# Kernel optimization log

Measured on AMD Instinct MI355X. Metric: run time of the kernel, lower is better.

## Reference

```python
import jax, jax.numpy as jnp
import numpy as np

B, S, D = 32, 2048, 1024
H = 8
D_ATTN = 256
D_HEAD = D_ATTN // H          # 32
D_HEAD_OUT = D // H           # 128
SOFTMAX_TEMP = 1.0


def setup_inputs() -> dict:
    key = jax.random.key(0)
    k0, k1, k2, k3, k4 = jax.random.split(key, 5)
    features = jax.random.normal(k0, (B, S, D), dtype=jnp.float32)
    # truncated-normal(std=0.01) init approximated with scaled normal
    w1 = jax.random.normal(k1, (H, D, D_HEAD), dtype=jnp.float32) * 0.01
    b1 = jax.random.normal(k2, (H, D_HEAD), dtype=jnp.float32) * 0.01
    w2 = jax.random.normal(k3, (H, D_HEAD, D_HEAD_OUT), dtype=jnp.float32) * 0.01
    b2 = jax.random.normal(k4, (H, D_HEAD_OUT), dtype=jnp.float32) * 0.01
    return {"features": features, "w1": w1, "b1": b1, "w2": w2, "b2": b2}


def reference(features, w1, b1, w2, b2):
    Bc, Sc, Dc = features.shape
    # per-head first projection: [B,H,S,d_head]
    h = jnp.einsum('bsd,hde->bhse', features, w1) + b1[None, :, None, :]
    h = jax.nn.gelu(h, approximate=False)  # torch nn.GELU default is exact erf
    # second projection: [B,H,S,d_head_out]
    logits = jnp.einsum('bhse,heo->bhso', h, w2) + b2[None, :, None, :]
    # softmax over seq dim (axis=2)
    smw = jax.nn.softmax(logits / SOFTMAX_TEMP, axis=2)
    # [B,H,S,D/H] -> [B,S,H,D/H] -> [B,S,D]
    smw = smw.transpose(0, 2, 1, 3).reshape(Bc, Sc, Dc)
    return (features * smw).sum(axis=1)  # [B,D]
```

## Files before the change

### kernel.cpp

```cpp
#include <hip/hip_runtime.h>
#include <hip/hip_bf16.h>
#include <math.h>

#define S_  2048
#define D_  1024

typedef __attribute__((ext_vector_type(8))) short short8;
typedef __attribute__((ext_vector_type(4))) float f32x4;

static __device__ __forceinline__ short f2bf(float x) {
    return __builtin_bit_cast(short, __float2bfloat16(x));
}
static __device__ __forceinline__ float bf2f(unsigned short s) {
    unsigned int u = ((unsigned int)s) << 16;
    return __builtin_bit_cast(float, u);
}

__device__ __forceinline__ void gl_lds16(const void* g, void* l) {
    __builtin_amdgcn_global_load_lds(
        (const __attribute__((address_space(1))) unsigned int*)g,
        (__attribute__((address_space(3))) unsigned int*)l, 16, 0, 0);
}

__global__ void prep_w1(const float* __restrict__ w1, short* __restrict__ w1p) {
    int tid = blockIdx.x * 256 + threadIdx.x;
    int lane = tid & 63;
    int fragid = tid >> 6;
    int cf = fragid & 15, ks = fragid >> 4;
    int col = cf * 16 + (lane & 15);
    int h = col >> 5, e = col & 31;
    int d0 = ks * 32 + (lane >> 4) * 8;
    short8 v;
#pragma unroll
    for (int r = 0; r < 8; ++r)
        v[r] = f2bf(w1[((size_t)h * D_ + (d0 + r)) * 32 + e]);
    *(short8*)(w1p + (size_t)tid * 8) = v;
}

__global__ void prep_w2(const float* __restrict__ w2, short* __restrict__ w2p) {
    int tid = blockIdx.x * 256 + threadIdx.x;
    int lane = tid & 63;
    int fragid = tid >> 6;
    int cf2 = fragid & 7, h = fragid >> 3;
    int o = cf2 * 16 + (lane & 15);
    int e0 = (lane >> 4) * 8;
    short8 v;
#pragma unroll
    for (int r = 0; r < 8; ++r)
        v[r] = f2bf(w2[((size_t)h * 32 + (e0 + r)) * 128 + o]);
    *(short8*)(w2p + (size_t)tid * 8) = v;
}

__global__ __launch_bounds__(256, 2) void gemm1(
        const float* __restrict__ feat,
        const short* __restrict__ w1p,
        const float* __restrict__ b1,
        short* __restrict__ hact)
{
    __shared__ short hstage[4][32][264];

    const int tid = threadIdx.x;
    const int wv = tid >> 6;
    const int lane = tid & 63;
    const int lr = lane & 15;
    const int lg = lane >> 4;
    const size_t mw = ((size_t)blockIdx.x * 4 + wv) * 32;

    const f32x4* A0 = (const f32x4*)(feat + (mw + lr) * D_);
    const f32x4* A1 = (const f32x4*)(feat + (mw + 16 + lr) * D_);
    const short8* Bp = (const short8*)w1p;

    const f32x4 vzero = {0.f, 0.f, 0.f, 0.f};
    f32x4 acc[2][16];
#pragma unroll
    for (int i = 0; i < 2; ++i)
#pragma unroll
        for (int j = 0; j < 16; ++j) acc[i][j] = vzero;

    f32x4 p0 = A0[lg * 2], p1 = A0[lg * 2 + 1];
    f32x4 p2 = A1[lg * 2], p3 = A1[lg * 2 + 1];

    for (int ks = 0; ks < 32; ++ks) {
        short8 af0, af1;
        af0[0] = f2bf(p0.x); af0[1] = f2bf(p0.y); af0[2] = f2bf(p0.z); af0[3] = f2bf(p0.w);
        af0[4] = f2bf(p1.x); af0[5] = f2bf(p1.y); af0[6] = f2bf(p1.z); af0[7] = f2bf(p1.w);
        af1[0] = f2bf(p2.x); af1[1] = f2bf(p2.y); af1[2] = f2bf(p2.z); af1[3] = f2bf(p2.w);
        af1[4] = f2bf(p3.x); af1[5] = f2bf(p3.y); af1[6] = f2bf(p3.z); af1[7] = f2bf(p3.w);
        if (ks < 31) {
            const int o = (ks + 1) * 8 + lg * 2;
            p0 = A0[o]; p1 = A0[o + 1];
            p2 = A1[o]; p3 = A1[o + 1];
        }
        const short8* Bk = Bp + (size_t)ks * 16 * 64 + lane;
#pragma unroll
        for (int cf = 0; cf < 16; ++cf) {
            short8 b = Bk[cf * 64];
            acc[0][cf] = __builtin_amdgcn_mfma_f32_16x16x32_bf16(af0, b, acc[0][cf], 0, 0, 0);
            acc[1][cf] = __builtin_amdgcn_mfma_f32_16x16x32_bf16(af1, b, acc[1][cf], 0, 0, 0);
        }
    }

#pragma unroll
    for (int cf = 0; cf < 16; ++cf) {
        const int col = cf * 16 + lr;
        const float bias = b1[col];
#pragma unroll
        for (int a = 0; a < 2; ++a)
#pragma unroll
        for (int r = 0; r < 4; ++r) {
            const int row = a * 16 + lg * 4 + r;
            float x = acc[a][cf][r] + bias;
            float g = 0.5f * x * (1.0f + erff(x * 0.70710678118654752f));
            hstage[wv][row][col] = f2bf(g);
        }
    }
#pragma unroll
    for (int it = 0; it < 16; ++it) {
        const int idx = it * 64 + lane;
        const int row = idx >> 5;
        const int c8 = idx & 31;
        short8 v = *(const short8*)(&hstage[wv][row][c8 * 8]);
        *(short8*)(hact + (mw + row) * 256 + c8 * 8) = v;
    }
}

__global__ __launch_bounds__(256) void gemm2w(
        const short* __restrict__ hact,
        const float* __restrict__ feat,
        const short* __restrict__ w2p,
        const float* __restrict__ b2,
        float* __restrict__ pnum,
        float* __restrict__ pden)
{
    __shared__ __align__(16) char lds[41216];
    short* hstage = (short*)lds;
    unsigned short* Est = (unsigned short*)(lds + 8192);

    const int tid = threadIdx.x;
    const int wv = tid >> 6;
    const int lane = tid & 63;
    const int lr = lane & 15;
    const int lg = lane >> 4;
    const size_t m0 = (size_t)blockIdx.x * 16;

#pragma unroll
    for (int j = 0; j < 2; ++j)
        gl_lds16(hact + m0 * 256 + (size_t)(j * 256 + tid) * 8,
                 hstage + (j * 256 + wv * 64) * 8);

    float bias2[16];
#pragma unroll
    for (int cf = 0; cf < 16; ++cf)
        bias2[cf] = b2[(2 * wv + (cf >> 3)) * 128 + (cf & 7) * 16 + lr];

    __syncthreads();

    short8 ah0 = *(const short8*)(hstage + lr * 256 + (2 * wv + 0) * 32 + lg * 8);
    short8 ah1 = *(const short8*)(hstage + lr * 256 + (2 * wv + 1) * 32 + lg * 8);
    const f32x4 vzero = {0.f, 0.f, 0.f, 0.f};
#pragma unroll
    for (int cf = 0; cf < 16; ++cf) {
        const int h = 2 * wv + (cf >> 3);
        short8 bw = *(const short8*)(w2p + ((size_t)(h * 8 + (cf & 7)) * 64 + lane) * 8);
        f32x4 c = vzero;
        c = __builtin_amdgcn_mfma_f32_16x16x32_bf16((cf < 8) ? ah0 : ah1, bw, c, 0, 0, 0);
        const int colL = wv * 256 + (cf >> 3) * 128 + (cf & 7) * 16 + lr;
#pragma unroll
        for (int r = 0; r < 4; ++r) {
            float e = __expf(c[r] + bias2[cf]);
            Est[(lg * 4 + r) * 1032 + colL] = (unsigned short)f2bf(e);
        }
    }
    __syncthreads();

    const int c0 = tid * 4;
    f32x4 nacc = vzero, dacc = vzero;
    const float* fb = feat + m0 * D_ + c0;
#pragma unroll
    for (int row = 0; row < 16; ++row) {
        f32x4 fv = *(const f32x4*)(fb + (size_t)row * D_);
        unsigned long long ev = *(const unsigned long long*)(Est + row * 1032 + c0);
        f32x4 e;
        e.x = bf2f((unsigned short)(ev));
        e.y = bf2f((unsigned short)(ev >> 16));
        e.z = bf2f((unsigned short)(ev >> 32));
        e.w = bf2f((unsigned short)(ev >> 48));
        dacc += e;
        nacc += fv * e;
    }
    const size_t pb = (size_t)blockIdx.x * 1024 + c0;
    *(f32x4*)(pnum + pb) = nacc;
    *(f32x4*)(pden + pb) = dacc;
}

__global__ __launch_bounds__(256) void finalize3(
        const float* __restrict__ pnum,
        const float* __restrict__ pden,
        float* __restrict__ out)
{
    const int idx = blockIdx.x * 256 + threadIdx.x;
    const int b = idx >> 10;
    const int d = idx & 1023;
    const size_t base = (size_t)b * 128 * 1024 + d;
    float n = 0.f, dn = 0.f;
    for (int j = 0; j < 128; ++j) {
        n  += pnum[base + (size_t)j * 1024];
        dn += pden[base + (size_t)j * 1024];
    }
    out[idx] = n / dn;
}

extern "C" void kernel_launch(void* const* d_in, const int* in_sizes, int n_in,
                              void* d_out, int out_size, void* d_ws, size_t ws_size,
                              hipStream_t stream) {
    (void)in_sizes; (void)n_in; (void)out_size; (void)ws_size;
    const float* feat = (const float*)d_in[0];
    const float* w1   = (const float*)d_in[1];
    const float* b1   = (const float*)d_in[2];
    const float* w2   = (const float*)d_in[3];
    const float* b2   = (const float*)d_in[4];
    float* out = (float*)d_out;

    char* ws = (char*)d_ws;
    short* hact = (short*)ws;
    float* pnum = (float*)(ws + (32ull << 20));
    float* pden = (float*)(ws + (48ull << 20));
    short* w1p  = (short*)(ws + (64ull << 20));
    short* w2p  = (short*)(ws + (64ull << 20) + (512ull << 10));

    prep_w1<<<128, 256, 0, stream>>>(w1, w1p);
    prep_w2<<<16, 256, 0, stream>>>(w2, w2p);
    gemm1<<<512, 256, 0, stream>>>(feat, w1p, b1, hact);
    gemm2w<<<4096, 256, 0, stream>>>(hact, feat, w2p, b2, pnum, pden);
    finalize3<<<128, 256, 0, stream>>>(pnum, pden, out);
}
```

Before: 211.2 us.

## Split gemm1 wave tiles across output columns to double grid size

gemm1 now gives each block 64 rows, with its four waves arranged 2x2. Each wave computes 32 rows by 128 of the 256 output columns instead of 32 rows by all columns, which halves the accumulator registers. The grid doubles to 1024 blocks and the min-blocks launch bound is dropped, aiming for more parallelism and occupancy on the GPU's compute units. In exchange, each feature row is now loaded and converted to bf16 by two waves instead of one, which doubles the A-side global reads and conversion work.

```diff
diff --git a/kernel.cpp b/kernel.cpp
--- a/kernel.cpp
+++ b/kernel.cpp
@@ -51,34 +51,39 @@
     *(short8*)(w2p + (size_t)tid * 8) = v;
 }
 
-__global__ __launch_bounds__(256, 2) void gemm1(
+__global__ __launch_bounds__(256) void gemm1(
         const float* __restrict__ feat,
         const short* __restrict__ w1p,
         const float* __restrict__ b1,
         short* __restrict__ hact)
 {
-    __shared__ short hstage[4][32][264];
+    __shared__ short hstage[4][32][136];
 
     const int tid = threadIdx.x;
     const int wv = tid >> 6;
     const int lane = tid & 63;
     const int lr = lane & 15;
     const int lg = lane >> 4;
-    const size_t mw = ((size_t)blockIdx.x * 4 + wv) * 32;
-
-    const f32x4* A0 = (const f32x4*)(feat + (mw + lr) * D_);
-    const f32x4* A1 = (const f32x4*)(feat + (mw + 16 + lr) * D_);
+    const int wr = wv >> 1, wc = wv & 1;
+    const size_t m0 = (size_t)blockIdx.x * 64;
+
+    const float* A0 = feat + (m0 + (size_t)(wr * 32 + lr)) * D_;
+    const float* A1 = feat + (m0 + (size_t)(wr * 32 + 16 + lr)) * D_;
     const short8* Bp = (const short8*)w1p;
 
     const f32x4 vzero = {0.f, 0.f, 0.f, 0.f};
-    f32x4 acc[2][16];
+    f32x4 acc[2][8];
 #pragma unroll
     for (int i = 0; i < 2; ++i)
 #pragma unroll
-        for (int j = 0; j < 16; ++j) acc[i][j] = vzero;
-
-    f32x4 p0 = A0[lg * 2], p1 = A0[lg * 2 + 1];
-    f32x4 p2 = A1[lg * 2], p3 = A1[lg * 2 + 1];
+        for (int j = 0; j < 8; ++j) acc[i][j] = vzero;
+
+    f32x4 p0, p1, p2, p3;
+    {
+        const int o = lg * 8;
+        p0 = *(const f32x4*)(A0 + o); p1 = *(const f32x4*)(A0 + o + 4);
+        p2 = *(const f32x4*)(A1 + o); p3 = *(const f32x4*)(A1 + o + 4);
+    }
 
     for (int ks = 0; ks < 32; ++ks) {
         short8 af0, af1;
@@ -87,22 +92,22 @@
         af1[0] = f2bf(p2.x); af1[1] = f2bf(p2.y); af1[2] = f2bf(p2.z); af1[3] = f2bf(p2.w);
         af1[4] = f2bf(p3.x); af1[5] = f2bf(p3.y); af1[6] = f2bf(p3.z); af1[7] = f2bf(p3.w);
         if (ks < 31) {
-            const int o = (ks + 1) * 8 + lg * 2;
-            p0 = A0[o]; p1 = A0[o + 1];
-            p2 = A1[o]; p3 = A1[o + 1];
-        }
-        const short8* Bk = Bp + (size_t)ks * 16 * 64 + lane;
-#pragma unroll
-        for (int cf = 0; cf < 16; ++cf) {
-            short8 b = Bk[cf * 64];
-            acc[0][cf] = __builtin_amdgcn_mfma_f32_16x16x32_bf16(af0, b, acc[0][cf], 0, 0, 0);
-            acc[1][cf] = __builtin_amdgcn_mfma_f32_16x16x32_bf16(af1, b, acc[1][cf], 0, 0, 0);
-        }
-    }
-
-#pragma unroll
-    for (int cf = 0; cf < 16; ++cf) {
-        const int col = cf * 16 + lr;
+            const int o = (ks + 1) * 32 + lg * 8;
+            p0 = *(const f32x4*)(A0 + o); p1 = *(const f32x4*)(A0 + o + 4);
+            p2 = *(const f32x4*)(A1 + o); p3 = *(const f32x4*)(A1 + o + 4);
+        }
+        const short8* Bk = Bp + (size_t)ks * 1024 + (wc * 8) * 64 + lane;
+#pragma unroll
+        for (int j = 0; j < 8; ++j) {
+            short8 b = Bk[j * 64];
+            acc[0][j] = __builtin_amdgcn_mfma_f32_16x16x32_bf16(af0, b, acc[0][j], 0, 0, 0);
+            acc[1][j] = __builtin_amdgcn_mfma_f32_16x16x32_bf16(af1, b, acc[1][j], 0, 0, 0);
+        }
+    }
+
+#pragma unroll
+    for (int cf = 0; cf < 8; ++cf) {
+        const int col = wc * 128 + cf * 16 + lr;
         const float bias = b1[col];
 #pragma unroll
         for (int a = 0; a < 2; ++a)
@@ -111,16 +116,16 @@
             const int row = a * 16 + lg * 4 + r;
             float x = acc[a][cf][r] + bias;
             float g = 0.5f * x * (1.0f + erff(x * 0.70710678118654752f));
-            hstage[wv][row][col] = f2bf(g);
-        }
-    }
-#pragma unroll
-    for (int it = 0; it < 16; ++it) {
+            hstage[wv][row][cf * 16 + lr] = f2bf(g);
+        }
+    }
+#pragma unroll
+    for (int it = 0; it < 8; ++it) {
         const int idx = it * 64 + lane;
-        const int row = idx >> 5;
-        const int c8 = idx & 31;
+        const int row = idx >> 4;
+        const int c8 = idx & 15;
         short8 v = *(const short8*)(&hstage[wv][row][c8 * 8]);
-        *(short8*)(hact + (mw + row) * 256 + c8 * 8) = v;
+        *(short8*)(hact + (m0 + (size_t)(wr * 32 + row)) * 256 + wc * 128 + c8 * 8) = v;
     }
 }
 
@@ -230,7 +235,7 @@
 
     prep_w1<<<128, 256, 0, stream>>>(w1, w1p);
     prep_w2<<<16, 256, 0, stream>>>(w2, w2p);
-    gemm1<<<512, 256, 0, stream>>>(feat, w1p, b1, hact);
+    gemm1<<<1024, 256, 0, stream>>>(feat, w1p, b1, hact);
     gemm2w<<<4096, 256, 0, stream>>>(hact, feat, w2p, b2, pnum, pden);
     finalize3<<<128, 256, 0, stream>>>(pnum, pden, out);
 }
```

Measured after the change: 217.2 us. 2.8% more time.
